# Kernel tuning notes

Hardware: AMD Instinct MI355X
Metric: run time of the kernel (lower is better)

The kernel has to match this reference:

```python
import jax, jax.numpy as jnp
import numpy as np

B, C, H, W = 8, 192, 128, 128
NUM_HEADS = 4
EPS = 1e-12  # torch F.normalize default eps


def _conv(x, w, groups=1):
    # NCHW conv, stride 1, SAME padding (kernel 1x1 or 3x3 with pad 1)
    return jax.lax.conv_general_dilated(
        x, w, window_strides=(1, 1), padding='SAME',
        dimension_numbers=('NCHW', 'OIHW', 'NCHW'),
        feature_group_count=groups)


def setup_inputs() -> dict:
    key = jax.random.key(0)
    ks = jax.random.split(key, 7)
    s = 0.02
    x = jax.random.normal(ks[0], (B, C, H, W), dtype=jnp.float32)
    cn = jax.random.normal(ks[1], (B, C, H, W), dtype=jnp.float32)
    cn_conv1_w = jax.random.normal(ks[2], (C, C, 1, 1), dtype=jnp.float32) * s
    cn_conv3_w = jax.random.normal(ks[3], (C, C, 3, 3), dtype=jnp.float32) * s
    qkv_w = jax.random.normal(ks[4], (3 * C, C, 1, 1), dtype=jnp.float32) * s
    qkv_dw_w = jax.random.normal(ks[5], (3 * C, 1, 3, 3), dtype=jnp.float32) * s
    proj_w = jax.random.normal(ks[6], (C, C, 1, 1), dtype=jnp.float32) * s
    temperature = jnp.ones((NUM_HEADS, 1, 1), dtype=jnp.float32)
    return {'x': x, 'cn': cn, 'cn_conv1_w': cn_conv1_w, 'cn_conv3_w': cn_conv3_w,
            'qkv_w': qkv_w, 'qkv_dw_w': qkv_dw_w, 'proj_w': proj_w,
            'temperature': temperature}


def reference(x, cn, cn_conv1_w, cn_conv3_w, qkv_w, qkv_dw_w, proj_w, temperature):
    b, c, h, w = x.shape
    ch = c // NUM_HEADS

    # color-naming feature branch: 1x1 conv then 3x3 conv
    cn_f = _conv(_conv(cn, cn_conv1_w), cn_conv3_w)

    # qkv: 1x1 conv then depthwise 3x3 conv (groups = 3*dim)
    qkv = _conv(_conv(x, qkv_w), qkv_dw_w, groups=3 * c)
    q, k, v = jnp.split(qkv, 3, axis=1)

    def to_heads(t):  # (b, c, h, w) -> (b, head, c/head, h*w)
        return t.reshape(b, NUM_HEADS, ch, h * w)

    def l2n(t):  # L2 normalize over spatial (last) dim, torch-style eps clamp
        return t / jnp.maximum(jnp.linalg.norm(t, axis=-1, keepdims=True), EPS)

    q = l2n(to_heads(q))
    k = l2n(to_heads(k))
    v = to_heads(v)
    cn_h = l2n(to_heads(cn_f))

    # cn_as_value=False, cn_only=False: q = normalize(q + normalized cn)
    q = l2n(q + cn_h)

    # transposed (channel) attention: [b, head, ch, ch]
    attn = jax.nn.softmax(jnp.einsum('bhcs,bhds->bhcd', q, k) * temperature, axis=-1)
    out = jnp.einsum('bhcd,bhds->bhcs', attn, v).reshape(b, c, h, w)
    return _conv(out, proj_w)
```

## Files before the change

### kernel.cpp

```cpp
#include <hip/hip_runtime.h>
#include <hip/hip_bf16.h>

typedef _Float16 f16;
typedef _Float16 f16x8 __attribute__((ext_vector_type(8)));
typedef float f32x4 __attribute__((ext_vector_type(4)));

#define NB 8
#define NC 192
#define NC3 576
#define NS 16384
#define NHD 4

#define OFF_X16   (0ll)
#define OFF_CN16  (50331648ll)
#define OFF_CN1   (100663296ll)
#define OFF_CNF   (150994944ll)
#define OFF_QKVD  (201326592ll)
#define OFF_NORMS (352321536ll)
#define OFF_G1    (352346112ll)
#define OFF_G2    (352641024ll)
#define OFF_ZPAD  (352935936ll)
#define OFF_ATTN  (352936960ll)
#define OFF_W116  (353231872ll)
#define OFF_WQ16  (353305600ll)
#define OFF_W3P   (353526784ll)
#define OFF_MCOMB (354190336ll)
#define OFF_WDWT  (354780160ll)
#define OFF_G1P   (100663296ll)
#define OFF_G2P   (110100480ll)
#define OFF_NPART (119537664ll)

__device__ __forceinline__ void async16(const void* g, void* l) {
  __builtin_amdgcn_global_load_lds(
      (const __attribute__((address_space(1))) unsigned int*)g,
      (__attribute__((address_space(3))) unsigned int*)l, 16, 0, 0);
}
#define MFMA(a,b,c) __builtin_amdgcn_mfma_f32_16x16x32_f16((a),(b),(c),0,0,0)

__global__ void k_wcast(const float* __restrict__ w1, const float* __restrict__ wq,
                        const float* __restrict__ w3, const float* __restrict__ wdw,
                        f16* __restrict__ w1o, f16* __restrict__ wqo,
                        f16* __restrict__ w3p, f16* __restrict__ wdwT)
{
  int idx = blockIdx.x * 256 + threadIdx.x;
  if (idx < 36864) {
    w1o[idx] = (f16)w1[idx];
  } else if (idx < 147456) {
    int i = idx - 36864;
    wqo[i] = (f16)wq[i];
  } else if (idx < 479232) {
    int i = idx - 147456;
    int tap = i / 36864;
    int rem = i % 36864;
    w3p[i] = (f16)w3[(size_t)rem * 9 + tap];
  } else if (idx < 484416) {
    int i = idx - 479232;
    int tap = i / 576;
    int gc = i % 576;
    wdwT[i] = (f16)wdw[(size_t)gc * 9 + tap];
  }
}

__global__ __launch_bounds__(256)
void k_cast_t(const float* __restrict__ xin, const float* __restrict__ cnin,
              f16* __restrict__ xo, f16* __restrict__ cno)
{
  __shared__ f16 tile[64 * 66];
  int b = blockIdx.z & 7;
  const float* in = (blockIdx.z >= 8) ? cnin : xin;
  f16* out = (blockIdx.z >= 8) ? cno : xo;
  int s0 = blockIdx.x * 64, c0 = blockIdx.y * 64;
  int t = threadIdx.x;
  int sl = t & 63, cq = t >> 6;
#pragma unroll
  for (int r = 0; r < 16; ++r) {
    int cl = r * 4 + cq;
    float v = in[((size_t)b * NC + c0 + cl) * NS + s0 + sl];
    tile[cl * 66 + sl] = (f16)v;
  }
  __syncthreads();
  int cl2 = t & 63, sq = t >> 6;
#pragma unroll
  for (int r = 0; r < 16; ++r) {
    int sl2 = r * 4 + sq;
    out[((size_t)b * NS + s0 + sl2) * NC + c0 + cl2] = tile[cl2 * 66 + sl2];
  }
}

__global__ __launch_bounds__(256, 2)
void k_gemm_act(const f16* __restrict__ act, const f16* __restrict__ wt,
                f16* __restrict__ out)
{
  __shared__ f16 At[256 * 32];
  __shared__ f16 Bt[64 * 32];
  const int tid = threadIdx.x;
  const int b = blockIdx.z;
  const int s0 = blockIdx.x * 256;
  const int n0 = blockIdx.y * 64;
  const int w = tid >> 6, lane = tid & 63, quad = lane >> 4, l16 = lane & 15;
  const f16* actB = act + (size_t)b * NS * NC;

  const f32x4 Z = {0.f, 0.f, 0.f, 0.f};
  f32x4 acc[4][4];
#pragma unroll
  for (int i = 0; i < 4; ++i)
#pragma unroll
    for (int j = 0; j < 4; ++j) acc[i][j] = Z;

  for (int kc = 0; kc < 6; ++kc) {
    const int k0 = kc * 32;
#pragma unroll
    for (int i = 0; i < 4; ++i) {
      int r = i * 64 + (w << 4) + (lane >> 2);
      int col = k0 + ((((lane & 3) + (r >> 2)) & 3) << 3);
      async16(actB + (size_t)(s0 + r) * NC + col, At + (size_t)(i * 64 + (w << 4)) * 32);
    }
    {
      int rb = (w << 4) + (lane >> 2);
      int colb = k0 + ((((lane & 3) + (rb >> 2)) & 3) << 3);
      async16(wt + (size_t)(n0 + rb) * NC + colb, Bt + (size_t)(w << 4) * 32);
    }
    __syncthreads();

    f16x8 bf[4];
#pragma unroll
    for (int nt = 0; nt < 4; ++nt) {
      int n = nt * 16 + l16;
      int p = (quad - (n >> 2)) & 3;
      bf[nt] = *(const f16x8*)(Bt + n * 32 + p * 8);
    }
#pragma unroll
    for (int mt = 0; mt < 4; ++mt) {
      int m = w * 64 + mt * 16 + l16;
      int p = (quad - (m >> 2)) & 3;
      f16x8 af = *(const f16x8*)(At + m * 32 + p * 8);
#pragma unroll
      for (int nt = 0; nt < 4; ++nt) acc[mt][nt] = MFMA(af, bf[nt], acc[mt][nt]);
    }
    __syncthreads();
  }
#pragma unroll
  for (int mt = 0; mt < 4; ++mt)
#pragma unroll
    for (int r = 0; r < 4; ++r) {
      int sg = s0 + w * 64 + mt * 16 + quad * 4 + r;
      f16* o = out + ((size_t)b * NS + sg) * NC + n0;
#pragma unroll
      for (int nt = 0; nt < 4; ++nt) o[nt * 16 + l16] = (f16)acc[mt][nt][r];
    }
}

__global__ __launch_bounds__(256, 2)
void k_conv3(const f16* __restrict__ act, const f16* __restrict__ w3p,
             f16* __restrict__ out, const f16* __restrict__ zpad)
{
  __shared__ f16 At[4 * 130 * 32];
  __shared__ f16 Bt[5 * 64 * 32];
  const int tid = threadIdx.x;
  const int bid = blockIdx.x;
  const int swz = (bid & 7) * 192 + (bid >> 3);
  const int b = swz / 192;
  const int rem = swz % 192;
  const int stile = rem / 3;
  const int nblk = rem % 3;
  const int y0 = stile * 2;
  const int s0 = stile * 256;
  const int n0 = nblk * 64;
  const int w = tid >> 6, lane = tid & 63, quad = lane >> 4, l16 = lane & 15;
  const f16* actB = act + (size_t)b * NS * NC;

  {
    int pos = tid >> 5, ch = tid & 31;
    At[((pos >> 1) * 130 + ((pos & 1) ? 129 : 0)) * 32 + ch] = (f16)0.f;
  }

  const f32x4 Z = {0.f, 0.f, 0.f, 0.f};
  f32x4 acc[4][4];
#pragma unroll
  for (int i = 0; i < 4; ++i)
#pragma unroll
    for (int j = 0; j < 4; ++j) acc[i][j] = Z;

  const int yrow = y0 - 1 + w;
  const bool rowok = ((unsigned)yrow < 128u);
  const f16* arow = actB + (size_t)(yrow * 128) * NC;

  for (int kc = 0; kc < 6; ++kc) {
    const int k0 = kc * 32;
#pragma unroll
    for (int i = 0; i < 8; ++i) {
      int x = i * 16 + (lane >> 2);
      int rs = w * 130 + 1 + x;
      int gsrc = ((lane & 3) + (rs >> 2)) & 3;
      const f16* g = rowok ? (arow + (size_t)x * NC + k0 + gsrc * 8)
                           : (const f16*)zpad;
      async16(g, At + (w * 130 + 1) * 32 + i * 512);
    }
#pragma unroll
    for (int tp = 0; tp < 5; ++tp) {
      int co = (w << 4) + (lane >> 2);
      int gsrc = ((lane & 3) + (co >> 2)) & 3;
      async16(w3p + (size_t)tp * NC * NC + (size_t)(n0 + co) * NC + k0 + gsrc * 8,
              Bt + (tp * 64 + (w << 4)) * 32);
    }
    __syncthreads();
#pragma unroll
    for (int tp = 0; tp < 5; ++tp) {
      const int dy = tp / 3 - 1, dx = tp % 3 - 1;
      f16x8 bf[4];
#pragma unroll
      for (int nt = 0; nt < 4; ++nt) {
        int n = nt * 16 + l16;
        int p = (quad - (n >> 2)) & 3;
        bf[nt] = *(const f16x8*)(Bt + (tp * 64 + n) * 32 + p * 8);
      }
#pragma unroll
      for (int mt = 0; mt < 4; ++mt) {
        int m = (w << 6) + mt * 16 + l16;
        int rr = ((m >> 7) + 1 + dy) * 130 + (m & 127) + 1 + dx;
        int p = (quad - (rr >> 2)) & 3;
        f16x8 af = *(const f16x8*)(At + rr * 32 + p * 8);
#pragma unroll
        for (int nt = 0; nt < 4; ++nt) acc[mt][nt] = MFMA(af, bf[nt], acc[mt][nt]);
      }
    }
    __syncthreads();
#pragma unroll
    for (int tp = 0; tp < 4; ++tp) {
      int co = (w << 4) + (lane >> 2);
      int gsrc = ((lane & 3) + (co >> 2)) & 3;
      async16(w3p + (size_t)(tp + 5) * NC * NC + (size_t)(n0 + co) * NC + k0 + gsrc * 8,
              Bt + (tp * 64 + (w << 4)) * 32);
    }
    __syncthreads();
#pragma unroll
    for (int tp = 0; tp < 4; ++tp) {
      const int tap = tp + 5;
      const int dy = tap / 3 - 1, dx = tap % 3 - 1;
      f16x8 bf[4];
#pragma unroll
      for (int nt = 0; nt < 4; ++nt) {
        int n = nt * 16 + l16;
        int p = (quad - (n >> 2)) & 3;
        bf[nt] = *(const f16x8*)(Bt + (tp * 64 + n) * 32 + p * 8);
      }
#pragma unroll
      for (int mt = 0; mt < 4; ++mt) {
        int m = (w << 6) + mt * 16 + l16;
        int rr = ((m >> 7) + 1 + dy) * 130 + (m & 127) + 1 + dx;
        int p = (quad - (rr >> 2)) & 3;
        f16x8 af = *(const f16x8*)(At + rr * 32 + p * 8);
#pragma unroll
        for (int nt = 0; nt < 4; ++nt) acc[mt][nt] = MFMA(af, bf[nt], acc[mt][nt]);
      }
    }
    __syncthreads();
  }
#pragma unroll
  for (int mt = 0; mt < 4; ++mt)
#pragma unroll
    for (int r = 0; r < 4; ++r) {
      int sg = s0 + (w << 6) + mt * 16 + quad * 4 + r;
      f16* o = out + ((size_t)b * NS + sg) * NC + n0;
#pragma unroll
      for (int nt = 0; nt < 4; ++nt) o[nt * 16 + l16] = (f16)acc[mt][nt][r];
    }
}

__global__ __launch_bounds__(256)
void k_dw(const f16* __restrict__ in, const f16* __restrict__ wdwT,
          f16* __restrict__ out, int part)
{
  int idx = blockIdx.x * 256 + threadIdx.x;
  int cg = idx % 24;
  int s = (idx / 24) % NS;
  int b = idx / (24 * NS);
  int x = s & 127, y = s >> 7;
  const f16* ip = in + ((size_t)b * NS + s) * NC + cg * 8;
  const f16* wp = wdwT + part * NC + cg * 8;
  float a[8] = {0.f, 0.f, 0.f, 0.f, 0.f, 0.f, 0.f, 0.f};
#pragma unroll
  for (int t = 0; t < 9; ++t) {
    int dy = t / 3 - 1, dx = t % 3 - 1;
    if (((unsigned)(x + dx) < 128u) && ((unsigned)(y + dy) < 128u)) {
      f16x8 v = *(const f16x8*)(ip + (dy * 128 + dx) * NC);
      f16x8 wv = *(const f16x8*)(wp + t * NC3);
#pragma unroll
      for (int j = 0; j < 8; ++j) a[j] += (float)wv[j] * (float)v[j];
    }
  }
  f16x8 o;
#pragma unroll
  for (int j = 0; j < 8; ++j) o[j] = (f16)a[j];
  *(f16x8*)(out + ((size_t)b * NS + s) * NC3 + part * NC + cg * 8) = o;
}

__global__ __launch_bounds__(64)
void k_e2(const f16* __restrict__ qkvd, const f16* __restrict__ cnf,
          float* __restrict__ G1p, float* __restrict__ G2p,
          float* __restrict__ npart)
{
  __shared__ f16 qT[48 * 72];
  __shared__ f16 kT[48 * 72];
  __shared__ f16 cT[48 * 72];
  int blk = blockIdx.x;
  int split = blk & 31;
  int h = (blk >> 5) & 3;
  int b = blk >> 7;
  int lane = threadIdx.x, quad = lane >> 4, l16 = lane & 15;
  const f32x4 Z = {0.f, 0.f, 0.f, 0.f};
  f32x4 g1[3][3], g2[3][3];
#pragma unroll
  for (int i = 0; i < 3; ++i)
#pragma unroll
    for (int j = 0; j < 3; ++j) { g1[i][j] = Z; g2[i][j] = Z; }
  float q2[3] = {0.f, 0.f, 0.f}, k2[3] = {0.f, 0.f, 0.f};
  float cn2[3] = {0.f, 0.f, 0.f}, qc[3] = {0.f, 0.f, 0.f};

  int sBase = split * 512;
  for (int chunk = 0; chunk < 8; ++chunk) {
    int sb = sBase + chunk * 64;
    const f16* qrow = qkvd + ((size_t)b * NS + sb + lane) * NC3 + h * 48;
    const f16* crow = cnf + ((size_t)b * NS + sb + lane) * NC + h * 48;
    f16x8 qv[6], kv[6], nv[6];
#pragma unroll
    for (int i = 0; i < 6; ++i) {
      qv[i] = *(const f16x8*)(qrow + i * 8);
      kv[i] = *(const f16x8*)(qrow + 192 + i * 8);
      nv[i] = *(const f16x8*)(crow + i * 8);
    }
    __syncthreads();
#pragma unroll
    for (int i = 0; i < 6; ++i)
#pragma unroll
      for (int j = 0; j < 8; ++j) {
        int c = i * 8 + j;
        qT[c * 72 + lane] = qv[i][j];
        kT[c * 72 + lane] = kv[i][j];
        cT[c * 72 + lane] = nv[i][j];
      }
    __syncthreads();
#pragma unroll
    for (int kk = 0; kk < 2; ++kk) {
      int ko = kk * 32 + quad * 8;
      f16x8 bfr[3];
#pragma unroll
      for (int dt = 0; dt < 3; ++dt) {
        bfr[dt] = *(const f16x8*)(kT + (dt * 16 + l16) * 72 + ko);
#pragma unroll
        for (int j = 0; j < 8; ++j) { float kf = (float)bfr[dt][j]; k2[dt] += kf * kf; }
      }
#pragma unroll
      for (int ct = 0; ct < 3; ++ct) {
        f16x8 aq = *(const f16x8*)(qT + (ct * 16 + l16) * 72 + ko);
        f16x8 an = *(const f16x8*)(cT + (ct * 16 + l16) * 72 + ko);
#pragma unroll
        for (int j = 0; j < 8; ++j) {
          float qf = (float)aq[j], nf = (float)an[j];
          q2[ct] += qf * qf; cn2[ct] += nf * nf; qc[ct] += qf * nf;
        }
#pragma unroll
        for (int dt = 0; dt < 3; ++dt) {
          g1[ct][dt] = MFMA(aq, bfr[dt], g1[ct][dt]);
          g2[ct][dt] = MFMA(an, bfr[dt], g2[ct][dt]);
        }
      }
    }
  }
  size_t gbase = ((size_t)((b * NHD + h) * 32 + split)) * 2304;
#pragma unroll
  for (int ct = 0; ct < 3; ++ct)
#pragma unroll
    for (int dt = 0; dt < 3; ++dt)
#pragma unroll
      for (int r = 0; r < 4; ++r) {
        int c = ct * 16 + quad * 4 + r;
        int d = dt * 16 + l16;
        G1p[gbase + c * 48 + d] = g1[ct][dt][r];
        G2p[gbase + c * 48 + d] = g2[ct][dt][r];
      }
#pragma unroll
  for (int t = 0; t < 3; ++t) {
    q2[t] += __shfl_xor(q2[t], 16, 64);  q2[t] += __shfl_xor(q2[t], 32, 64);
    k2[t] += __shfl_xor(k2[t], 16, 64);  k2[t] += __shfl_xor(k2[t], 32, 64);
    cn2[t] += __shfl_xor(cn2[t], 16, 64); cn2[t] += __shfl_xor(cn2[t], 32, 64);
    qc[t] += __shfl_xor(qc[t], 16, 64);  qc[t] += __shfl_xor(qc[t], 32, 64);
  }
  if (lane < 16) {
#pragma unroll
    for (int ct = 0; ct < 3; ++ct) {
      int c = h * 48 + ct * 16 + lane;
      float* np = npart + (((size_t)(b * 32 + split)) * NC + c) * 4;
      np[0] = q2[ct]; np[1] = k2[ct]; np[2] = cn2[ct]; np[3] = qc[ct];
    }
  }
}

__global__ void k_e1b(const float* __restrict__ npart, float* __restrict__ norms)
{
  int idx = blockIdx.x * 256 + threadIdx.x;
  int b = idx / 768;
  int cs = idx % 768;
  const float* p = npart + (size_t)b * 32 * 768 + cs;
  float s = 0.f;
#pragma unroll
  for (int sp = 0; sp < 32; ++sp) s += p[sp * 768];
  norms[idx] = s;
}

__global__ void k_e2b(const float* __restrict__ G1p, const float* __restrict__ G2p,
                      float* __restrict__ G1, float* __restrict__ G2)
{
  int idx = blockIdx.x * 256 + threadIdx.x;
  int bh = idx / 2304;
  int cd = idx % 2304;
  const float* p1 = G1p + ((size_t)bh * 32) * 2304 + cd;
  const float* p2 = G2p + ((size_t)bh * 32) * 2304 + cd;
  float s1 = 0.f, s2 = 0.f;
#pragma unroll
  for (int sp = 0; sp < 32; ++sp) { s1 += p1[sp * 2304]; s2 += p2[sp * 2304]; }
  G1[idx] = s1;
  G2[idx] = s2;
}

__global__ __launch_bounds__(64)
void k_f1(const float* __restrict__ G1, const float* __restrict__ G2,
          const float* __restrict__ norms, const float* __restrict__ temp,
          float* __restrict__ attn)
{
  __shared__ float S[48 * 48];
  int h = blockIdx.x & 3, b = blockIdx.x >> 2;
  int t = threadIdx.x;
  float T = temp[h];
  const float EPS = 1e-12f;
#pragma unroll
  for (int i = 0; i < 36; ++i) {
    int idx = i * 64 + t;
    int c = idx / 48, d = idx % 48;
    const float* np = norms + ((size_t)b * NC + h * 48 + c) * 4;
    float q2 = np[0], cn2 = np[2], qc = np[3];
    float nq = fmaxf(sqrtf(q2), EPS);
    float ncn = fmaxf(sqrtf(cn2), EPS);
    float k2 = norms[((size_t)b * NC + h * 48 + d) * 4 + 1];
    float nk = fmaxf(sqrtf(k2), EPS);
    float ss = q2 / (nq * nq) + 2.f * qc / (nq * ncn) + cn2 / (ncn * ncn);
    float nsum = fmaxf(sqrtf(fmaxf(ss, 0.f)), EPS);
    size_t go = (((size_t)(b * NHD + h) * 48 + c) * 48 + d);
    S[idx] = (G1[go] / nq + G2[go] / ncn) / (nsum * nk) * T;
  }
  __syncthreads();
  if (t < 48) {
    float mx = -1e30f;
    for (int d = 0; d < 48; ++d) mx = fmaxf(mx, S[t * 48 + d]);
    float sum = 0.f;
    for (int d = 0; d < 48; ++d) { float e = expf(S[t * 48 + d] - mx); S[t * 48 + d] = e; sum += e; }
    float inv = 1.f / sum;
    float* ap = attn + (((size_t)(b * NHD + h) * 48 + t) * 48);
    for (int d = 0; d < 48; ++d) ap[d] = S[t * 48 + d] * inv;
  }
}

__global__ void k_f2(const float* __restrict__ attn, const float* __restrict__ projw,
                     f16* __restrict__ mcomb)
{
  int idx = blockIdx.x * 256 + threadIdx.x;
  int dg = idx % NC;
  int co = (idx / NC) % NC;
  int b = idx / (NC * NC);
  int h = dg / 48, dl = dg % 48;
  const float* pw = projw + (size_t)co * NC + h * 48;
  const float* at = attn + ((size_t)(b * NHD + h) * 48) * 48 + dl;
  float a = 0.f;
#pragma unroll
  for (int cl = 0; cl < 48; ++cl) a += pw[cl] * at[cl * 48];
  mcomb[idx] = (f16)a;
}

__global__ __launch_bounds__(256, 2)
void k_gemm_out(const f16* __restrict__ mcomb, const f16* __restrict__ qkvd,
                float* __restrict__ out)
{
  __shared__ f16 At[64 * 32];
  __shared__ f16 Bt[256 * 32];
  const int tid = threadIdx.x;
  const int b = blockIdx.z;
  const int s0 = blockIdx.x * 256;
  const int m0 = blockIdx.y * 64;
  const int w = tid >> 6, lane = tid & 63, quad = lane >> 4, l16 = lane & 15;
  const f16* mcB = mcomb + (size_t)b * NC * NC;
  const f16* vB = qkvd + (size_t)b * NS * NC3 + 384;

  const f32x4 Z = {0.f, 0.f, 0.f, 0.f};
  f32x4 acc[4][4];
#pragma unroll
  for (int i = 0; i < 4; ++i)
#pragma unroll
    for (int j = 0; j < 4; ++j) acc[i][j] = Z;

  for (int kc = 0; kc < 6; ++kc) {
    const int k0 = kc * 32;
    {
      int rb = (w << 4) + (lane >> 2);
      int colb = k0 + ((((lane & 3) + (rb >> 2)) & 3) << 3);
      async16(mcB + (size_t)(m0 + rb) * NC + colb, At + (size_t)(w << 4) * 32);
    }
#pragma unroll
    for (int i = 0; i < 4; ++i) {
      int r = i * 64 + (w << 4) + (lane >> 2);
      int col = k0 + ((((lane & 3) + (r >> 2)) & 3) << 3);
      async16(vB + (size_t)(s0 + r) * NC3 + col, Bt + (size_t)(i * 64 + (w << 4)) * 32);
    }
    __syncthreads();
    f16x8 af[4];
#pragma unroll
    for (int mt = 0; mt < 4; ++mt) {
      int m = mt * 16 + l16;
      int p = (quad - (m >> 2)) & 3;
      af[mt] = *(const f16x8*)(At + m * 32 + p * 8);
    }
#pragma unroll
    for (int nt = 0; nt < 4; ++nt) {
      int n = w * 64 + nt * 16 + l16;
      int p = (quad - (n >> 2)) & 3;
      f16x8 bf = *(const f16x8*)(Bt + n * 32 + p * 8);
#pragma unroll
      for (int mt = 0; mt < 4; ++mt) acc[mt][nt] = MFMA(af[mt], bf, acc[mt][nt]);
    }
    __syncthreads();
  }
#pragma unroll
  for (int mt = 0; mt < 4; ++mt)
#pragma unroll
    for (int r = 0; r < 4; ++r) {
      int cog = m0 + mt * 16 + quad * 4 + r;
      float* o = out + ((size_t)b * NC + cog) * NS + s0 + w * 64;
#pragma unroll
      for (int nt = 0; nt < 4; ++nt) o[nt * 16 + l16] = acc[mt][nt][r];
    }
}

extern "C" void kernel_launch(void* const* d_in, const int* in_sizes, int n_in,
                              void* d_out, int out_size, void* d_ws, size_t ws_size,
                              hipStream_t stream) {
  const float* x   = (const float*)d_in[0];
  const float* cn  = (const float*)d_in[1];
  const float* w1  = (const float*)d_in[2];
  const float* w3  = (const float*)d_in[3];
  const float* wq  = (const float*)d_in[4];
  const float* wdw = (const float*)d_in[5];
  const float* wpj = (const float*)d_in[6];
  const float* tmp = (const float*)d_in[7];
  float* out = (float*)d_out;
  char* ws = (char*)d_ws;

  f16* x16    = (f16*)(ws + OFF_X16);
  f16* cn16   = (f16*)(ws + OFF_CN16);
  f16* qkv1p  = (f16*)(ws + OFF_CN16);
  f16* cn1    = (f16*)(ws + OFF_CN1);
  f16* cnf    = (f16*)(ws + OFF_CNF);
  f16* qkvd   = (f16*)(ws + OFF_QKVD);
  float* norms = (float*)(ws + OFF_NORMS);
  float* G1    = (float*)(ws + OFF_G1);
  float* G2    = (float*)(ws + OFF_G2);
  f16* zpad   = (f16*)(ws + OFF_ZPAD);
  float* attn  = (float*)(ws + OFF_ATTN);
  f16* w116   = (f16*)(ws + OFF_W116);
  f16* wq16   = (f16*)(ws + OFF_WQ16);
  f16* w3p    = (f16*)(ws + OFF_W3P);
  f16* mcomb  = (f16*)(ws + OFF_MCOMB);
  f16* wdwT   = (f16*)(ws + OFF_WDWT);
  float* G1p   = (float*)(ws + OFF_G1P);
  float* G2p   = (float*)(ws + OFF_G2P);
  float* npart = (float*)(ws + OFF_NPART);

  hipMemsetAsync(ws + OFF_ZPAD, 0, 1024, stream);

  k_wcast<<<1893, 256, 0, stream>>>(w1, wq, w3, wdw, w116, wq16, w3p, wdwT);
  k_cast_t<<<dim3(256, 3, 16), 256, 0, stream>>>(x, cn, x16, cn16);
  k_gemm_act<<<dim3(64, 3, 8), 256, 0, stream>>>(cn16, w116, cn1);
  k_conv3<<<1536, 256, 0, stream>>>(cn1, w3p, cnf, zpad);
  for (int p = 0; p < 3; ++p) {
    k_gemm_act<<<dim3(64, 3, 8), 256, 0, stream>>>(x16, wq16 + p * 36864, qkv1p);
    k_dw<<<12288, 256, 0, stream>>>(qkv1p, wdwT, qkvd, p);
  }
  k_e2<<<1024, 64, 0, stream>>>(qkvd, cnf, G1p, G2p, npart);
  k_e1b<<<24, 256, 0, stream>>>(npart, norms);
  k_e2b<<<1152, 256, 0, stream>>>(G1p, G2p, G1, G2);
  k_f1<<<32, 64, 0, stream>>>(G1, G2, norms, tmp, attn);
  k_f2<<<1152, 256, 0, stream>>>(attn, wpj, mcomb);
  k_gemm_out<<<dim3(64, 3, 8), 256, 0, stream>>>(mcomb, qkvd, out);

  (void)in_sizes; (void)n_in; (void)out_size; (void)ws_size;
}
```

Baseline: 705.5 us.

## Fuse fp32-to-fp16 cast and transpose into the 1x1 conv GEMM load

Removes the separate cast/transpose kernel. The 1x1 GEMM now reads fp32 NCHW activations directly, converts them to fp16 in registers and writes them transposed into shared memory. This saves a full write and re-read of two 8x192x16384 half-precision tensors. In exchange, the x input is re-read and re-converted for each of the three qkv passes and for each of the three N-tiles. The block index is also flattened so that the batch index varies fastest, and one barrier per k-step is dropped in favour of a sync placed before the shared-memory stores.

Result: faster. 672.8 us (-4.6%).

```diff
diff --git a/kernel.cpp b/kernel.cpp
--- a/kernel.cpp
+++ b/kernel.cpp
@@ -2,6 +2,7 @@
 #include <hip/hip_bf16.h>
 
 typedef _Float16 f16;
+typedef _Float16 f16x4 __attribute__((ext_vector_type(4)));
 typedef _Float16 f16x8 __attribute__((ext_vector_type(8)));
 typedef float f32x4 __attribute__((ext_vector_type(4)));
 
@@ -61,44 +62,22 @@
   }
 }
 
-__global__ __launch_bounds__(256)
-void k_cast_t(const float* __restrict__ xin, const float* __restrict__ cnin,
-              f16* __restrict__ xo, f16* __restrict__ cno)
-{
-  __shared__ f16 tile[64 * 66];
-  int b = blockIdx.z & 7;
-  const float* in = (blockIdx.z >= 8) ? cnin : xin;
-  f16* out = (blockIdx.z >= 8) ? cno : xo;
-  int s0 = blockIdx.x * 64, c0 = blockIdx.y * 64;
-  int t = threadIdx.x;
-  int sl = t & 63, cq = t >> 6;
-#pragma unroll
-  for (int r = 0; r < 16; ++r) {
-    int cl = r * 4 + cq;
-    float v = in[((size_t)b * NC + c0 + cl) * NS + s0 + sl];
-    tile[cl * 66 + sl] = (f16)v;
-  }
-  __syncthreads();
-  int cl2 = t & 63, sq = t >> 6;
-#pragma unroll
-  for (int r = 0; r < 16; ++r) {
-    int sl2 = r * 4 + sq;
-    out[((size_t)b * NS + s0 + sl2) * NC + c0 + cl2] = tile[cl2 * 66 + sl2];
-  }
-}
-
 __global__ __launch_bounds__(256, 2)
-void k_gemm_act(const f16* __restrict__ act, const f16* __restrict__ wt,
-                f16* __restrict__ out)
+void k_gemm_tc(const float* __restrict__ actf, const f16* __restrict__ wt,
+               f16* __restrict__ out)
 {
   __shared__ f16 At[256 * 32];
   __shared__ f16 Bt[64 * 32];
   const int tid = threadIdx.x;
-  const int b = blockIdx.z;
-  const int s0 = blockIdx.x * 256;
-  const int n0 = blockIdx.y * 64;
+  const int bid = blockIdx.x;
+  const int b = bid & 7;
+  const int rem = bid >> 3;
+  const int s0 = (rem / 3) * 256;
+  const int n0 = (rem % 3) * 64;
   const int w = tid >> 6, lane = tid & 63, quad = lane >> 4, l16 = lane & 15;
-  const f16* actB = act + (size_t)b * NS * NC;
+  const int sb = lane;
+  const int cb = w;
+  const float* actB = actf + ((size_t)b * NC) * NS + s0 + 4 * sb;
 
   const f32x4 Z = {0.f, 0.f, 0.f, 0.f};
   f32x4 acc[4][4];
@@ -109,17 +88,24 @@
 
   for (int kc = 0; kc < 6; ++kc) {
     const int k0 = kc * 32;
-#pragma unroll
-    for (int i = 0; i < 4; ++i) {
-      int r = i * 64 + (w << 4) + (lane >> 2);
-      int col = k0 + ((((lane & 3) + (r >> 2)) & 3) << 3);
-      async16(actB + (size_t)(s0 + r) * NC + col, At + (size_t)(i * 64 + (w << 4)) * 32);
-    }
+    const float* ap = actB + (size_t)(k0 + cb * 8) * NS;
+    f32x4 r[8];
+#pragma unroll
+    for (int rr = 0; rr < 8; ++rr) r[rr] = *(const f32x4*)(ap + (size_t)rr * NS);
+    __syncthreads();
     {
       int rb = (w << 4) + (lane >> 2);
       int colb = k0 + ((((lane & 3) + (rb >> 2)) & 3) << 3);
       async16(wt + (size_t)(n0 + rb) * NC + colb, Bt + (size_t)(w << 4) * 32);
     }
+    const int cp = (cb - sb) & 3;
+#pragma unroll
+    for (int j = 0; j < 4; ++j) {
+      f16x8 o;
+#pragma unroll
+      for (int rr = 0; rr < 8; ++rr) o[rr] = (f16)r[rr][j];
+      *(f16x8*)(At + (4 * sb + j) * 32 + cp * 8) = o;
+    }
     __syncthreads();
 
     f16x8 bf[4];
@@ -137,7 +123,6 @@
 #pragma unroll
       for (int nt = 0; nt < 4; ++nt) acc[mt][nt] = MFMA(af, bf[nt], acc[mt][nt]);
     }
-    __syncthreads();
   }
 #pragma unroll
   for (int mt = 0; mt < 4; ++mt)
@@ -553,8 +538,6 @@
   float* out = (float*)d_out;
   char* ws = (char*)d_ws;
 
-  f16* x16    = (f16*)(ws + OFF_X16);
-  f16* cn16   = (f16*)(ws + OFF_CN16);
   f16* qkv1p  = (f16*)(ws + OFF_CN16);
   f16* cn1    = (f16*)(ws + OFF_CN1);
   f16* cnf    = (f16*)(ws + OFF_CNF);
@@ -576,11 +559,10 @@
   hipMemsetAsync(ws + OFF_ZPAD, 0, 1024, stream);
 
   k_wcast<<<1893, 256, 0, stream>>>(w1, wq, w3, wdw, w116, wq16, w3p, wdwT);
-  k_cast_t<<<dim3(256, 3, 16), 256, 0, stream>>>(x, cn, x16, cn16);
-  k_gemm_act<<<dim3(64, 3, 8), 256, 0, stream>>>(cn16, w116, cn1);
+  k_gemm_tc<<<1536, 256, 0, stream>>>(cn, w116, cn1);
   k_conv3<<<1536, 256, 0, stream>>>(cn1, w3p, cnf, zpad);
   for (int p = 0; p < 3; ++p) {
-    k_gemm_act<<<dim3(64, 3, 8), 256, 0, stream>>>(x16, wq16 + p * 36864, qkv1p);
+    k_gemm_tc<<<1536, 256, 0, stream>>>(x, wq16 + p * 36864, qkv1p);
     k_dw<<<12288, 256, 0, stream>>>(qkv1p, wdwT, qkvd, p);
   }
   k_e2<<<1024, 64, 0, stream>>>(qkvd, cnf, G1p, G2p, npart);
```
